# Performance work log

Hardware: AMD Instinct MI355X
Metric: run time of the kernel (lower is better)

## Reference

```python
import jax, jax.numpy as jnp
import numpy as np

B, NMAX, D, NUM = 1024, 128, 256, 4
EPS = 1e-8
NEG = -1e9


def segment_softmax(logits, seg):
    # torch_geometric-style softmax over ragged segments. logits: (T,)
    m = jax.ops.segment_max(logits, seg, num_segments=B)
    e = jnp.exp(logits - m[seg])
    s = jax.ops.segment_sum(e, seg, num_segments=B)
    return e / (s[seg] + 1e-16)


def to_dense(v, seg, pos):
    # scatter ragged rows into (B, NMAX, ...) dense batch
    return jnp.zeros((B, NMAX) + v.shape[1:], v.dtype).at[seg, pos].set(v)


def uot_badmm(x, q0d, maskf, a1, a2, a3, rho):
    # Bregman-ADMM solver for entropic unbalanced OT (f_method='badmm-e').
    # x: (B,N,D) cost (to be maximized); q0d, maskf: (B,N,1); a1,a2,a3,rho: (NUM,)
    log_p0 = jnp.full((B, 1, D), -jnp.log(float(D)), x.dtype)  # uniform dim prior
    log_q0 = jnp.log(q0d + EPS)                                # (B,N,1)
    log_t = log_q0 + log_p0                                    # T init = q0 p0^T
    log_s = log_t
    log_mu = log_p0
    log_eta = log_q0
    z = jnp.zeros_like(x)
    z1 = jnp.zeros_like(log_p0)
    z2 = jnp.zeros_like(log_q0)
    neg = (1.0 - maskf) * NEG  # exclude padded rows from N-axis softmax
    for k in range(NUM):
        r, b1, b2, b3 = rho[k], a1[k], a2[k], a3[k]
        # T-update: rows (over D) sum to eta
        y = (x - z + r * log_s) / (b2 + r)
        log_t = log_eta + jax.nn.log_softmax(y, axis=2)
        # S-update: columns (over N) sum to mu, masked
        y = (z + r * log_t) / (b1 + r) + neg
        log_s = log_mu + jax.nn.log_softmax(y, axis=1)
        # unbalanced marginal updates (KL to priors, weight a3)
        log_mu = (b3 * log_p0 - z1 + r * jax.nn.logsumexp(log_s, axis=1, keepdims=True)) / (b3 + r)
        log_eta = (b3 * log_q0 - z2 + r * jax.nn.logsumexp(log_t, axis=2, keepdims=True)) / (b3 + r)
        # dual ascent
        t = jnp.exp(log_t) * maskf
        s = jnp.exp(log_s) * maskf
        z = z + r * (t - s)
        z1 = z1 + r * (jnp.exp(log_mu) - jnp.sum(s, axis=1, keepdims=True))
        z2 = z2 + r * (jnp.exp(log_eta) - jnp.sum(t, axis=2, keepdims=True)) * maskf
    return jnp.exp(log_t) * maskf


def setup_inputs() -> dict:
    rng = np.random.default_rng(0)
    lengths = rng.integers(NMAX // 2, NMAX + 1, size=B)
    lengths[0] = NMAX  # ensure max size present
    batch = jnp.asarray(np.repeat(np.arange(B), lengths), dtype=jnp.int32)
    total = int(lengths.sum())
    ks = jax.random.split(jax.random.key(0), 8)
    x = jax.random.normal(ks[0], (total, D), jnp.float32)
    W1 = jax.random.normal(ks[1], (2 * D, D), jnp.float32) / np.float32(np.sqrt(D))
    W2 = jax.random.normal(ks[2], (1, 2 * D), jnp.float32) / np.float32(np.sqrt(2 * D))
    rho = 0.1 * jax.random.normal(ks[3], (NUM,), jnp.float32)
    a1 = 0.1 * jax.random.normal(ks[4], (NUM,), jnp.float32)
    a2 = 0.1 * jax.random.normal(ks[5], (NUM,), jnp.float32)
    a3 = 0.1 * jax.random.normal(ks[6], (NUM,), jnp.float32)
    return {"x": x, "batch": batch, "W1": W1, "W2": W2, "rho": rho, "a1": a1, "a2": a2, "a3": a3}


def reference(x, batch, W1, W2, rho, a1, a2, a3):
    # attention-based sample prior q0 (q0 != 'fixed' branch)
    h = jnp.tanh(x @ W1.T)          # (T, 2D)
    logits = (h @ W2.T)[:, 0]       # (T,)
    q0 = segment_softmax(logits, batch)[:, None]  # (T, 1)
    # ragged -> dense batch (to_dense_batch)
    counts = jax.ops.segment_sum(jnp.ones_like(batch), batch, num_segments=B)
    starts = jnp.cumsum(counts) - counts
    pos = jnp.arange(batch.shape[0]) - starts[batch]
    xd = to_dense(x, batch, pos)    # (B, NMAX, D)
    q0d = to_dense(q0, batch, pos)  # (B, NMAX, 1)
    mask = to_dense(jnp.ones((batch.shape[0], 1), x.dtype), batch, pos)  # (B, NMAX, 1)
    trans = uot_badmm(xd, q0d, mask,
                      jax.nn.softplus(a1), jax.nn.softplus(a2),
                      jax.nn.softplus(a3), jax.nn.softplus(rho))
    frot = D * xd * trans * mask    # (B, NMAX, D)
    return jnp.sum(frot, axis=1)    # (B, D)
```

## Files before the change

kernel.cpp:

```cpp
#include <hip/hip_runtime.h>
#include <math.h>

#define BB   1024
#define DD   256
#define LOGD 5.5451774444795624753f
#define RST  260

typedef __attribute__((ext_vector_type(8))) short short8;
typedef __attribute__((ext_vector_type(4))) float f32x4;

__device__ __forceinline__ float wave_sum(float v){
  #pragma unroll
  for (int off=32; off>0; off>>=1) v += __shfl_xor(v, off, 64);
  return v;
}
__device__ __forceinline__ float wave_max(float v){
  #pragma unroll
  for (int off=32; off>0; off>>=1) v = fmaxf(v, __shfl_xor(v, off, 64));
  return v;
}
__device__ __forceinline__ float grp_sum(float v){
  v += __shfl_xor(v, 1, 64);
  v += __shfl_xor(v, 2, 64);
  v += __shfl_xor(v, 4, 64);
  v += __shfl_xor(v, 8, 64);
  return v;
}
__device__ __forceinline__ float fast_tanh(float x){
  return 1.0f - 2.0f/(__expf(2.0f*x)+1.0f);
}
__device__ __forceinline__ unsigned short f2bf(float f){
  unsigned int u = __float_as_uint(f);
  unsigned int r = u + 0x7FFFu + ((u >> 16) & 1u);
  return (unsigned short)(r >> 16);
}
__device__ __forceinline__ float decq(int q16){ return (float)q16 * (1.0f/512.0f); }
__device__ __forceinline__ int   zenc(float z){
  float t = fmaf(z, 4096.0f, 12582912.0f);
  return __float_as_int(t) - 0x4B400000;
}
__device__ __forceinline__ float zdec(int q){ return (float)q * (1.0f/4096.0f); }
__device__ __forceinline__ int lo16(unsigned u){ return ((int)(u<<16))>>16; }
__device__ __forceinline__ int hi16(unsigned u){ return ((int)u)>>16; }
__device__ __forceinline__ unsigned pk2(int a, int b){
  return ((unsigned)a & 0xffffu) | ((unsigned)b << 16);
}
__device__ __forceinline__ unsigned pkadd_sat(unsigned a, unsigned b){
  unsigned d; asm("v_pk_add_i16 %0, %1, %2 clamp" : "=v"(d) : "v"(a), "v"(b)); return d;
}

__global__ void k_pre(const float* __restrict__ W1, unsigned short* __restrict__ w1b,
                      const int* __restrict__ batch, int T, int* __restrict__ starts,
                      const float* __restrict__ rho, const float* __restrict__ a1,
                      const float* __restrict__ a2, const float* __restrict__ a3,
                      float* __restrict__ P)
{
  const int blk = blockIdx.x, tid = threadIdx.x;
  if (blk < 64){
    const int t = blk*256 + tid;
    #pragma unroll
    for (int i=0;i<2;i++){
      const int idx = (t*2 + i)*4;
      const float4 v = *(const float4*)(W1 + idx);
      *(ushort4*)(w1b + idx) = make_ushort4(f2bf(v.x), f2bf(v.y), f2bf(v.z), f2bf(v.w));
    }
  } else if (blk < 69){
    const int b = (blk-64)*256 + tid;
    if (b <= BB){
      int lo = 0, hi = T;
      while (lo < hi){ int mid = (lo+hi)>>1; if (batch[mid] < b) lo = mid+1; else hi = mid; }
      starts[b] = lo;
    }
  } else if (tid == 0){
    float lm = -LOGD, z1 = 0.f;
    for (int k=0;k<4;k++){
      float r  = log1pf(expf(rho[k]));
      float b1 = log1pf(expf(a1[k]));
      float b2 = log1pf(expf(a2[k]));
      float b3 = log1pf(expf(a3[k]));
      P[k]    = r;
      P[4+k]  = 1.f/(b1+r);
      P[8+k]  = 1.f/(b2+r);
      P[12+k] = lm;
      P[16+k] = b3;
      P[20+k] = 1.f/(b3+r);
      float lmn = (b3*(-LOGD) - z1 + r*lm)/(b3+r);
      z1 += r*(expf(lmn)-expf(lm));
      lm = lmn;
    }
  }
}

#define LPW 72
__global__ __launch_bounds__(512, 2) void k_mlp(
    const float* __restrict__ x, const unsigned short* __restrict__ w1b,
    const float* __restrict__ W2, float* __restrict__ logits, int T)
{
  __shared__ unsigned short Xs[128*LPW];
  __shared__ unsigned short Ws[128*LPW];
  __shared__ float lred[128];
  const int by = blockIdx.x;
  const int bx = blockIdx.y;
  const int tid = threadIdx.x;
  if (tid < 128) lred[tid] = 0.f;

  const int l = tid & 63;
  const int w = tid >> 6;
  const int wm = w >> 2;
  const int wn = w & 3;
  const int lr = l & 15, quad = l >> 4;
  const int srow = tid >> 2;
  const int sseg = tid & 3;
  const int wrow = tid >> 3;
  const int wseg = tid & 7;

  f32x4 acc[4][2];
  #pragma unroll
  for (int mi=0;mi<4;mi++)
    #pragma unroll
    for (int ni=0;ni<2;ni++) acc[mi][ni] = (f32x4){0.f,0.f,0.f,0.f};

  for (int kt=0; kt<4; kt++){
    const int k0 = kt*64;
    {
      const int grow = bx*128 + srow;
      #pragma unroll
      for (int i=0;i<4;i++){
        float4 v = make_float4(0.f,0.f,0.f,0.f);
        if (grow < T) v = *(const float4*)(x + (size_t)grow*DD + k0 + sseg*16 + i*4);
        *(ushort4*)&Xs[srow*LPW + sseg*16 + i*4] =
            make_ushort4(f2bf(v.x), f2bf(v.y), f2bf(v.z), f2bf(v.w));
      }
    }
    #pragma unroll
    for (int h=0; h<2; h++){
      const int r = h*64 + wrow;
      *(short8*)&Ws[r*LPW + wseg*8] =
          *(const short8*)(w1b + (size_t)(by*128 + r)*DD + k0 + wseg*8);
    }
    __syncthreads();
    #pragma unroll
    for (int ks=0; ks<2; ks++){
      short8 afr[4], bfr[2];
      #pragma unroll
      for (int mi=0;mi<4;mi++)
        afr[mi] = *(const short8*)&Xs[(wm*64 + mi*16 + lr)*LPW + ks*32 + quad*8];
      #pragma unroll
      for (int ni=0;ni<2;ni++)
        bfr[ni] = *(const short8*)&Ws[(wn*32 + ni*16 + lr)*LPW + ks*32 + quad*8];
      #pragma unroll
      for (int mi=0;mi<4;mi++)
        #pragma unroll
        for (int ni=0;ni<2;ni++)
          acc[mi][ni] = __builtin_amdgcn_mfma_f32_16x16x32_bf16(afr[mi], bfr[ni], acc[mi][ni], 0, 0, 0);
    }
    __syncthreads();
  }

  float w2v[2];
  #pragma unroll
  for (int ni=0;ni<2;ni++) w2v[ni] = W2[by*128 + wn*32 + ni*16 + lr];
  #pragma unroll
  for (int mi=0;mi<4;mi++){
    float p[4];
    #pragma unroll
    for (int v=0; v<4; v++){
      p[v] = fast_tanh(acc[mi][0][v])*w2v[0] + fast_tanh(acc[mi][1][v])*w2v[1];
      #pragma unroll
      for (int off=1; off<16; off<<=1) p[v] += __shfl_xor(p[v], off, 64);
    }
    if (lr == 0){
      #pragma unroll
      for (int v=0; v<4; v++)
        atomicAdd(&lred[wm*64 + mi*16 + quad*4 + v], p[v]);
    }
  }
  __syncthreads();
  if (tid < 128){
    const int grow = bx*128 + tid;
    if (grow < T) atomicAdd(logits + grow, lred[tid]);
  }
}

__global__ __launch_bounds__(512, 4) void k_solver(
    const float* __restrict__ x, const float* __restrict__ logits,
    const int* __restrict__ starts, const float* __restrict__ P,
    float* __restrict__ out)
{
  __shared__ __align__(16) float red[32*RST];
  __shared__ __align__(16) float colv[DD];
  const int b = blockIdx.x;
  const int start = starts[b];
  const int len = starts[b+1] - start;
  const int tid = threadIdx.x;
  const int w = tid >> 6, l = tid & 63;
  const int sub = l >> 4;
  const int c0  = l & 15;
  const int n0 = w*16;
  int nv = len - n0; nv = nv < 0 ? 0 : (nv > 16 ? 16 : nv);

  const float r0=P[0], r1=P[1], r2=P[2], r3=P[3];
  const float i10=P[4], i11=P[5], i12=P[6];
  const float i20=P[8], i21=P[9], i22=P[10], i23=P[11];
  const float mu0=P[12], mu1=P[13], mu2=P[14];
  const float b30=P[16], b31=P[17], b32=P[18];
  const float e30=P[20], e31=P[21], e32=P[22];

  const float* lg = logits + start;
  float v0 = (l      < len) ? lg[l]    : -3.0e38f;
  float v1 = (l+64   < len) ? lg[l+64] : -3.0e38f;
  float sm = wave_max(fmaxf(v0,v1));
  float se0 = (l    < len) ? __expf(v0-sm) : 0.f;
  float se1 = (l+64 < len) ? __expf(v1-sm) : 0.f;
  float ssum0 = wave_sum(se0+se1);
  const float sinv = 1.f/(ssum0 + 1e-16f);
  const float esel = (n0 < 64) ? se0 : se1;

  float slqg[4], etag[4], z2g[4];
  uint2 ap[4][4];
  uint2 zp[4][4];
  #pragma unroll
  for (int g=0; g<4; g++){
    const int row = n0 + 4*g + sub;
    const float ev = __shfl(esel, row & 63, 64);
    const float lq = __logf(ev*sinv + 1e-8f);
    slqg[g] = lq; etag[g] = lq; z2g[g] = 0.f;
    #pragma unroll
    for (int q=0;q<4;q++){ zp[g][q].x = 0u; zp[g][q].y = 0u; }
  }

  const float* xbase = x + (size_t)(start + n0 + sub)*DD + 4*c0;

  {
    float sp[16];
    #pragma unroll
    for (int j=0;j<16;j++) sp[j]=0.f;
    #pragma unroll
    for (int g=0; g<4; g++){
      if (4*g + sub < nv){
        const float* xp = xbase + (size_t)(4*g)*DD;
        const float a0 = slqg[g] - LOGD;
        float ss = 0.f;
        #pragma unroll
        for (int q=0;q<4;q++){
          const float4 xv = *(const float4*)(xp + 64*q);
          const float xvv[4] = {xv.x, xv.y, xv.z, xv.w};
          int ny[4];
          #pragma unroll
          for (int j=0;j<4;j++){
            const float y = (xvv[j] + r0*a0) * i20;
            ss += __expf(y);
            ny[j] = __float2int_rn(y*512.f);
          }
          ap[0][q] = ap[0][q];
          ap[g][q].x = pk2(ny[0],ny[1]);
          ap[g][q].y = pk2(ny[2],ny[3]);
        }
        ss = grp_sum(ss);
        const float off = etag[g] - __logf(ss);
        const int offi = __float2int_rn(fmaxf(off, -56.f)*512.f);
        const unsigned offpk = pk2(offi, offi);
        #pragma unroll
        for (int q=0;q<4;q++){
          ap[g][q].x = pkadd_sat(ap[g][q].x, offpk);
          ap[g][q].y = pkadd_sat(ap[g][q].y, offpk);
          sp[4*q+0] += __expf((r0*decq(lo16(ap[g][q].x))) * i10);
          sp[4*q+1] += __expf((r0*decq(hi16(ap[g][q].x))) * i10);
          sp[4*q+2] += __expf((r0*decq(lo16(ap[g][q].y))) * i10);
          sp[4*q+3] += __expf((r0*decq(hi16(ap[g][q].y))) * i10);
        }
        const float en = (b30*slqg[g] - z2g[g] + r0*etag[g]) * e30;
        z2g[g] += r0*(__expf(en) - __expf(etag[g]));
        etag[g] = en;
      }
    }
    #pragma unroll
    for (int q=0;q<4;q++)
      *(float4*)&red[(4*w+sub)*RST + 64*q + 4*c0] =
          make_float4(sp[4*q], sp[4*q+1], sp[4*q+2], sp[4*q+3]);
  }
  __syncthreads();
  if (tid < DD){
    float s = 0.f;
    #pragma unroll
    for (int i=0;i<32;i++) s += red[i*RST + tid];
    colv[tid] = __logf(s);
  }
  __syncthreads();

  #pragma unroll
  for (int k=1;k<3;k++){
    const float rkm = (k==1)? r0 : r1;
    const float ib1m= (k==1)? i10 : i11;
    const float mum = (k==1)? mu0 : mu1;
    const float rk  = (k==1)? r1 : r2;
    const float ib1k= (k==1)? i11 : i12;
    const float ib2k= (k==1)? i21 : i22;
    const float b3k = (k==1)? b31 : b32;
    const float e3k = (k==1)? e31 : e32;
    float sp[16];
    #pragma unroll
    for (int j=0;j<16;j++) sp[j]=0.f;
    #pragma unroll
    for (int g=0; g<4; g++){
      if (4*g + sub < nv){
        const float* xp = xbase + (size_t)(4*g)*DD;
        float ss = 0.f;
        #pragma unroll
        for (int q=0;q<4;q++){
          const float4 lscq = *(const float4*)&colv[64*q + 4*c0];
          const float4 xv   = *(const float4*)(xp + 64*q);
          const float xvv[4]  = {xv.x, xv.y, xv.z, xv.w};
          const float lscv[4] = {lscq.x, lscq.y, lscq.z, lscq.w};
          const int aq[4] = {lo16(ap[g][q].x), hi16(ap[g][q].x),
                             lo16(ap[g][q].y), hi16(ap[g][q].y)};
          const int zq[4] = {lo16(zp[g][q].x), hi16(zp[g][q].x),
                             lo16(zp[g][q].y), hi16(zp[g][q].y)};
          int ny[4], nz[4];
          #pragma unroll
          for (int j=0;j<4;j++){
            const float lt = decq(aq[j]);
            float zf = zdec(zq[j]);
            const float ys  = (zf + rkm*lt) * ib1m;
            const float lsn = mum + ys - lscv[j];
            zf += rkm*(__expf(lt) - __expf(lsn));
            nz[j] = zenc(zf);
            const float y = (xvv[j] - zdec(nz[j]) + rk*lsn) * ib2k;
            ss += __expf(y);
            ny[j] = __float2int_rn(y*512.f);
          }
          ap[g][q].x = pk2(ny[0],ny[1]);
          ap[g][q].y = pk2(ny[2],ny[3]);
          zp[g][q].x = pk2(nz[0],nz[1]);
          zp[g][q].y = pk2(nz[2],nz[3]);
        }
        ss = grp_sum(ss);
        const float off = etag[g] - __logf(ss);
        const int offi = __float2int_rn(fmaxf(off, -56.f)*512.f);
        const unsigned offpk = pk2(offi, offi);
        #pragma unroll
        for (int q=0;q<4;q++){
          ap[g][q].x = pkadd_sat(ap[g][q].x, offpk);
          ap[g][q].y = pkadd_sat(ap[g][q].y, offpk);
          sp[4*q+0] += __expf((zdec(lo16(zp[g][q].x)) + rk*decq(lo16(ap[g][q].x))) * ib1k);
          sp[4*q+1] += __expf((zdec(hi16(zp[g][q].x)) + rk*decq(hi16(ap[g][q].x))) * ib1k);
          sp[4*q+2] += __expf((zdec(lo16(zp[g][q].y)) + rk*decq(lo16(ap[g][q].y))) * ib1k);
          sp[4*q+3] += __expf((zdec(hi16(zp[g][q].y)) + rk*decq(hi16(ap[g][q].y))) * ib1k);
        }
        const float en = (b3k*slqg[g] - z2g[g] + rk*etag[g]) * e3k;
        z2g[g] += rk*(__expf(en) - __expf(etag[g]));
        etag[g] = en;
      }
    }
    #pragma unroll
    for (int q=0;q<4;q++)
      *(float4*)&red[(4*w+sub)*RST + 64*q + 4*c0] =
          make_float4(sp[4*q], sp[4*q+1], sp[4*q+2], sp[4*q+3]);
    __syncthreads();
    if (tid < DD){
      float s = 0.f;
      #pragma unroll
      for (int i=0;i<32;i++) s += red[i*RST + tid];
      colv[tid] = __logf(s);
    }
    __syncthreads();
  }

  {
    float op[16];
    #pragma unroll
    for (int j=0;j<16;j++) op[j]=0.f;
    #pragma unroll
    for (int g=0; g<4; g++){
      if (4*g + sub < nv){
        const float* xp = xbase + (size_t)(4*g)*DD;
        float ey[16];
        float ss = 0.f;
        #pragma unroll
        for (int q=0;q<4;q++){
          const float4 lscq = *(const float4*)&colv[64*q + 4*c0];
          const float4 xv   = *(const float4*)(xp + 64*q);
          const float xvv[4]  = {xv.x, xv.y, xv.z, xv.w};
          const float lscv[4] = {lscq.x, lscq.y, lscq.z, lscq.w};
          const int aq[4] = {lo16(ap[g][q].x), hi16(ap[g][q].x),
                             lo16(ap[g][q].y), hi16(ap[g][q].y)};
          const int zq[4] = {lo16(zp[g][q].x), hi16(zp[g][q].x),
                             lo16(zp[g][q].y), hi16(zp[g][q].y)};
          #pragma unroll
          for (int j=0;j<4;j++){
            const float lt = decq(aq[j]);
            float zf = zdec(zq[j]);
            const float ys  = (zf + r2*lt) * i12;
            const float lsn = mu2 + ys - lscv[j];
            zf += r2*(__expf(lt) - __expf(lsn));
            const float y = (xvv[j] - zf + r3*lsn) * i23;
            const float e = __expf(y);
            ey[4*q+j] = e;
            ss += e;
          }
        }
        ss = grp_sum(ss);
        const float rs = __expf(etag[g]) / ss;
        #pragma unroll
        for (int q=0;q<4;q++){
          const float4 xv = *(const float4*)(xp + 64*q);
          op[4*q+0] += xv.x * ey[4*q+0] * rs;
          op[4*q+1] += xv.y * ey[4*q+1] * rs;
          op[4*q+2] += xv.z * ey[4*q+2] * rs;
          op[4*q+3] += xv.w * ey[4*q+3] * rs;
        }
      }
    }
    #pragma unroll
    for (int q=0;q<4;q++)
      *(float4*)&red[(4*w+sub)*RST + 64*q + 4*c0] =
          make_float4(op[4*q], op[4*q+1], op[4*q+2], op[4*q+3]);
    __syncthreads();
    if (tid < DD){
      float s = 0.f;
      #pragma unroll
      for (int i=0;i<32;i++) s += red[i*RST + tid];
      out[(size_t)b*DD + tid] = 256.0f * s;
    }
  }
}

extern "C" void kernel_launch(void* const* d_in, const int* in_sizes, int n_in,
                              void* d_out, int out_size, void* d_ws, size_t ws_size,
                              hipStream_t stream) {
  const float* x    = (const float*)d_in[0];
  const int*   batch= (const int*)d_in[1];
  const float* W1   = (const float*)d_in[2];
  const float* W2   = (const float*)d_in[3];
  const float* rho  = (const float*)d_in[4];
  const float* a1   = (const float*)d_in[5];
  const float* a2   = (const float*)d_in[6];
  const float* a3   = (const float*)d_in[7];
  float* out = (float*)d_out;
  const int T = in_sizes[1];

  float* logits = (float*)d_ws;
  int*   starts = (int*)(logits + T);
  float* P      = (float*)(starts + 1028);
  unsigned short* w1b = (unsigned short*)(P + 32);

  k_pre<<<70, 256, 0, stream>>>(W1, w1b, batch, T, starts, rho, a1, a2, a3, P);
  hipMemsetAsync(logits, 0, (size_t)T*sizeof(float), stream);
  k_mlp<<<dim3(4, (T+127)/128), 512, 0, stream>>>(x, w1b, W2, logits, T);
  k_solver<<<BB, 512, 0, stream>>>(x, logits, starts, P, out);
}
```

Before: 352.4 us.

## Loop over all hidden tiles per block in MLP, dropping memset and atomics

Result: slower. 383.6 us (+8.8%).

```diff
diff --git a/kernel.cpp b/kernel.cpp
--- a/kernel.cpp
+++ b/kernel.cpp
@@ -71,36 +71,39 @@
       while (lo < hi){ int mid = (lo+hi)>>1; if (batch[mid] < b) lo = mid+1; else hi = mid; }
       starts[b] = lo;
     }
-  } else if (tid == 0){
-    float lm = -LOGD, z1 = 0.f;
-    for (int k=0;k<4;k++){
-      float r  = log1pf(expf(rho[k]));
-      float b1 = log1pf(expf(a1[k]));
-      float b2 = log1pf(expf(a2[k]));
-      float b3 = log1pf(expf(a3[k]));
-      P[k]    = r;
-      P[4+k]  = 1.f/(b1+r);
-      P[8+k]  = 1.f/(b2+r);
-      P[12+k] = lm;
-      P[16+k] = b3;
-      P[20+k] = 1.f/(b3+r);
-      float lmn = (b3*(-LOGD) - z1 + r*lm)/(b3+r);
-      z1 += r*(expf(lmn)-expf(lm));
-      lm = lmn;
+  } else {
+    if (tid == 0){
+      float lm = -LOGD, z1 = 0.f;
+      for (int k=0;k<4;k++){
+        float r  = log1pf(expf(rho[k]));
+        float b1 = log1pf(expf(a1[k]));
+        float b2 = log1pf(expf(a2[k]));
+        float b3 = log1pf(expf(a3[k]));
+        P[k]    = r;
+        P[4+k]  = 1.f/(b1+r);
+        P[8+k]  = 1.f/(b2+r);
+        P[12+k] = lm;
+        P[16+k] = b3;
+        P[20+k] = 1.f/(b3+r);
+        float lmn = (b3*(-LOGD) - z1 + r*lm)/(b3+r);
+        z1 += r*(expf(lmn)-expf(lm));
+        lm = lmn;
+      }
     }
   }
 }
 
 #define LPW 72
-__global__ __launch_bounds__(512, 2) void k_mlp(
+#define XST 264
+__global__ __launch_bounds__(512) __attribute__((amdgpu_waves_per_eu(2, 4)))
+void k_mlp(
     const float* __restrict__ x, const unsigned short* __restrict__ w1b,
     const float* __restrict__ W2, float* __restrict__ logits, int T)
 {
-  __shared__ unsigned short Xs[128*LPW];
+  __shared__ unsigned short Xs[128*XST];
   __shared__ unsigned short Ws[128*LPW];
   __shared__ float lred[128];
-  const int by = blockIdx.x;
-  const int bx = blockIdx.y;
+  const int bx = blockIdx.x;
   const int tid = threadIdx.x;
   if (tid < 128) lred[tid] = 0.f;
 
@@ -109,80 +112,83 @@
   const int wm = w >> 2;
   const int wn = w & 3;
   const int lr = l & 15, quad = l >> 4;
-  const int srow = tid >> 2;
-  const int sseg = tid & 3;
   const int wrow = tid >> 3;
   const int wseg = tid & 7;
 
-  f32x4 acc[4][2];
-  #pragma unroll
-  for (int mi=0;mi<4;mi++)
-    #pragma unroll
-    for (int ni=0;ni<2;ni++) acc[mi][ni] = (f32x4){0.f,0.f,0.f,0.f};
-
-  for (int kt=0; kt<4; kt++){
-    const int k0 = kt*64;
-    {
-      const int grow = bx*128 + srow;
-      #pragma unroll
-      for (int i=0;i<4;i++){
-        float4 v = make_float4(0.f,0.f,0.f,0.f);
-        if (grow < T) v = *(const float4*)(x + (size_t)grow*DD + k0 + sseg*16 + i*4);
-        *(ushort4*)&Xs[srow*LPW + sseg*16 + i*4] =
-            make_ushort4(f2bf(v.x), f2bf(v.y), f2bf(v.z), f2bf(v.w));
-      }
-    }
-    #pragma unroll
-    for (int h=0; h<2; h++){
-      const int r = h*64 + wrow;
-      *(short8*)&Ws[r*LPW + wseg*8] =
-          *(const short8*)(w1b + (size_t)(by*128 + r)*DD + k0 + wseg*8);
-    }
-    __syncthreads();
-    #pragma unroll
-    for (int ks=0; ks<2; ks++){
-      short8 afr[4], bfr[2];
-      #pragma unroll
-      for (int mi=0;mi<4;mi++)
-        afr[mi] = *(const short8*)&Xs[(wm*64 + mi*16 + lr)*LPW + ks*32 + quad*8];
-      #pragma unroll
-      for (int ni=0;ni<2;ni++)
-        bfr[ni] = *(const short8*)&Ws[(wn*32 + ni*16 + lr)*LPW + ks*32 + quad*8];
-      #pragma unroll
-      for (int mi=0;mi<4;mi++)
+  {
+    const int r = tid >> 2;
+    const int s = tid & 3;
+    const int grow = bx*128 + r;
+    #pragma unroll 4
+    for (int i=0;i<16;i++){
+      float4 v = make_float4(0.f,0.f,0.f,0.f);
+      if (grow < T) v = *(const float4*)(x + (size_t)grow*DD + s*64 + i*4);
+      *(ushort4*)&Xs[r*XST + s*64 + i*4] =
+          make_ushort4(f2bf(v.x), f2bf(v.y), f2bf(v.z), f2bf(v.w));
+    }
+  }
+
+  for (int by=0; by<4; by++){
+    f32x4 acc[4][2];
+    #pragma unroll
+    for (int mi=0;mi<4;mi++)
+      #pragma unroll
+      for (int ni=0;ni<2;ni++) acc[mi][ni] = (f32x4){0.f,0.f,0.f,0.f};
+
+    for (int kt=0; kt<4; kt++){
+      #pragma unroll
+      for (int h=0; h<2; h++){
+        const int r = h*64 + wrow;
+        *(short8*)&Ws[r*LPW + wseg*8] =
+            *(const short8*)(w1b + (size_t)(by*128 + r)*DD + kt*64 + wseg*8);
+      }
+      __syncthreads();
+      #pragma unroll
+      for (int ks=0; ks<2; ks++){
+        short8 afr[4], bfr[2];
+        #pragma unroll
+        for (int mi=0;mi<4;mi++)
+          afr[mi] = *(const short8*)&Xs[(wm*64 + mi*16 + lr)*XST + kt*64 + ks*32 + quad*8];
         #pragma unroll
         for (int ni=0;ni<2;ni++)
-          acc[mi][ni] = __builtin_amdgcn_mfma_f32_16x16x32_bf16(afr[mi], bfr[ni], acc[mi][ni], 0, 0, 0);
-    }
-    __syncthreads();
-  }
-
-  float w2v[2];
-  #pragma unroll
-  for (int ni=0;ni<2;ni++) w2v[ni] = W2[by*128 + wn*32 + ni*16 + lr];
-  #pragma unroll
-  for (int mi=0;mi<4;mi++){
-    float p[4];
-    #pragma unroll
-    for (int v=0; v<4; v++){
-      p[v] = fast_tanh(acc[mi][0][v])*w2v[0] + fast_tanh(acc[mi][1][v])*w2v[1];
-      #pragma unroll
-      for (int off=1; off<16; off<<=1) p[v] += __shfl_xor(p[v], off, 64);
-    }
-    if (lr == 0){
-      #pragma unroll
-      for (int v=0; v<4; v++)
-        atomicAdd(&lred[wm*64 + mi*16 + quad*4 + v], p[v]);
+          bfr[ni] = *(const short8*)&Ws[(wn*32 + ni*16 + lr)*LPW + ks*32 + quad*8];
+        #pragma unroll
+        for (int mi=0;mi<4;mi++)
+          #pragma unroll
+          for (int ni=0;ni<2;ni++)
+            acc[mi][ni] = __builtin_amdgcn_mfma_f32_16x16x32_bf16(afr[mi], bfr[ni], acc[mi][ni], 0, 0, 0);
+      }
+      __syncthreads();
+    }
+
+    float w2v[2];
+    #pragma unroll
+    for (int ni=0;ni<2;ni++) w2v[ni] = W2[by*128 + wn*32 + ni*16 + lr];
+    #pragma unroll
+    for (int mi=0;mi<4;mi++){
+      float p[4];
+      #pragma unroll
+      for (int v=0; v<4; v++){
+        p[v] = fast_tanh(acc[mi][0][v])*w2v[0] + fast_tanh(acc[mi][1][v])*w2v[1];
+        #pragma unroll
+        for (int off=1; off<16; off<<=1) p[v] += __shfl_xor(p[v], off, 64);
+      }
+      if (lr == 0){
+        #pragma unroll
+        for (int v=0; v<4; v++)
+          atomicAdd(&lred[wm*64 + mi*16 + quad*4 + v], p[v]);
+      }
     }
   }
   __syncthreads();
   if (tid < 128){
     const int grow = bx*128 + tid;
-    if (grow < T) atomicAdd(logits + grow, lred[tid]);
-  }
-}
-
-__global__ __launch_bounds__(512, 4) void k_solver(
+    if (grow < T) logits[grow] = lred[tid];
+  }
+}
+
+__global__ __launch_bounds__(512) __attribute__((amdgpu_waves_per_eu(4, 6)))
+void k_solver(
     const float* __restrict__ x, const float* __restrict__ logits,
     const int* __restrict__ starts, const float* __restrict__ P,
     float* __restrict__ out)
@@ -252,7 +258,6 @@
             ss += __expf(y);
             ny[j] = __float2int_rn(y*512.f);
           }
-          ap[0][q] = ap[0][q];
           ap[g][q].x = pk2(ny[0],ny[1]);
           ap[g][q].y = pk2(ny[2],ny[3]);
         }
@@ -445,7 +450,6 @@
   unsigned short* w1b = (unsigned short*)(P + 32);
 
   k_pre<<<70, 256, 0, stream>>>(W1, w1b, batch, T, starts, rho, a1, a2, a3, P);
-  hipMemsetAsync(logits, 0, (size_t)T*sizeof(float), stream);
-  k_mlp<<<dim3(4, (T+127)/128), 512, 0, stream>>>(x, w1b, W2, logits, T);
+  k_mlp<<<(T+127)/128, 512, 0, stream>>>(x, w1b, W2, logits, T);
   k_solver<<<BB, 512, 0, stream>>>(x, logits, starts, P, out);
 }
```
